# Performance work log

Hardware: AMD Instinct MI355X
Metric: run time of the kernel (lower is better)

## Reference

```python
import jax, jax.numpy as jnp
import numpy as np

N_TRAIN, D, B, N_CLASSES, K = 50000, 64, 128, 10, 16


def setup_inputs() -> dict:
    key = jax.random.key(0)
    k1, k2, k3 = jax.random.split(key, 3)
    train_data = jax.random.normal(k1, (N_TRAIN, D), dtype=jnp.float32)
    # one-hot class labels, as implied by gather -> sum over k -> argmax over classes
    labels = jax.random.randint(k2, (N_TRAIN,), 0, N_CLASSES)
    train_target = jax.nn.one_hot(labels, N_CLASSES, dtype=jnp.float32)
    x_test = jax.random.normal(k3, (B, D), dtype=jnp.float32)
    return {"train_data": train_data, "train_target": train_target,
            "x_test": x_test, "k": K}


def reference(train_data, train_target, x_test, k):
    # L1 (Manhattan) distance: [B, N_train]
    # broadcast: [1, N, D] - [B, 1, D] -> abs -> sum over D
    distance = jnp.sum(jnp.abs(train_data[None, :, :] - x_test[:, None, :]), axis=2)
    # top_k of negative distance == k nearest neighbors
    _, top_k_indices = jax.lax.top_k(-distance, k)          # [B, k]
    top_k_label = train_target[top_k_indices]               # [B, k, C] gather
    sum_up_predictions = jnp.sum(top_k_label, axis=1)       # [B, C] vote counts
    return jnp.argmax(sum_up_predictions, axis=1)           # [B] predicted class
```

## Files before the change

### kernel.cpp

```cpp
#include <hip/hip_runtime.h>
#include <cfloat>
#include <climits>
#include <stdint.h>

#define NTRAIN 50000
#define DIM 64
#define BQ 128
#define NCLS 10
#define KSEL 16
#define QPB 32
#define QG (BQ / QPB)
#define THREADS 256
#define TROWS 256
#define TPAD 68

__device__ __forceinline__ uint64_t pack_di(float d, int r) {
    return ((uint64_t)__float_as_uint(d) << 32) | (uint32_t)r;
}

__device__ __forceinline__ void ins16(uint64_t (&K)[KSEL], uint64_t pk) {
    if (pk < K[KSEL - 1]) {
        K[KSEL - 1] = pk;
#pragma unroll
        for (int j = KSEL - 1; j > 0; --j)
            if (K[j] < K[j - 1]) { uint64_t t = K[j]; K[j] = K[j - 1]; K[j - 1] = t; }
    }
}

__device__ __forceinline__ uint64_t adv16(const uint64_t (&K)[KSEL], int c) {
    uint64_t nh = ~0ULL;
#pragma unroll
    for (int q = 1; q < KSEL; ++q)
        if (c == q) nh = K[q];
    return nh;
}

__device__ __forceinline__ void wave_merge8(const uint64_t (&K)[KSEL], int rg, uint64_t* dst) {
    uint64_t h = K[0]; int c = 0;
#pragma unroll
    for (int r = 0; r < KSEL; ++r) {
        uint64_t m = h, o;
        o = __shfl_xor((unsigned long long)m, 1); if (o < m) m = o;
        o = __shfl_xor((unsigned long long)m, 2); if (o < m) m = o;
        o = __shfl_xor((unsigned long long)m, 4); if (o < m) m = o;
        if (m == h) { ++c; h = adv16(K, c); }
        if (rg == (r & 7)) dst[r] = m;
    }
}

__global__ __launch_bounds__(THREADS, 1) void knn_scan(
    const float* __restrict__ train, const float* __restrict__ xtest,
    uint64_t* __restrict__ cand, int S, int stripe_len)
{
    __shared__ float qs[QPB * TPAD];
    __shared__ __align__(16) float ts[TROWS * TPAD];

    const int bx     = blockIdx.x;
    const int stripe = bx % S;
    const int qgrp   = bx / S;
    const int q0     = qgrp * QPB;
    const int tid    = threadIdx.x;
    const int w      = tid >> 6;
    const int lane   = tid & 63;
    const int qg     = lane >> 3;
    const int rg     = lane & 7;

    const int r0 = stripe * stripe_len;
    const int r1 = min(NTRAIN, r0 + stripe_len);

    for (int f = tid; f < QPB * (DIM / 4); f += THREADS) {
        const int ql = f >> 4, c = f & 15;
        *(float4*)&qs[ql * TPAD + 4 * c] =
            *(const float4*)&xtest[(size_t)(q0 + ql) * DIM + 4 * c];
    }

    uint64_t k0[KSEL], k1[KSEL], k2[KSEL], k3[KSEL];
#pragma unroll
    for (int j = 0; j < KSEL; ++j) { k0[j] = ~0ULL; k1[j] = ~0ULL; k2[j] = ~0ULL; k3[j] = ~0ULL; }

    for (int base = r0; base < r1; base += TROWS) {
        const int nr = min(TROWS, r1 - base);
        __syncthreads();
        for (int f = tid; f < nr * (DIM / 4); f += THREADS) {
            const int r = f >> 4, c = f & 15;
            *(float4*)&ts[r * TPAD + 4 * c] =
                *(const float4*)&train[(size_t)(base + r) * DIM + 4 * c];
        }
        __syncthreads();

        float acc[4][8];
#pragma unroll
        for (int i = 0; i < 4; ++i)
#pragma unroll
            for (int j = 0; j < 8; ++j) acc[i][j] = 0.0f;

#pragma unroll 4
        for (int c = 0; c < DIM / 4; ++c) {
            float4 qv[4], tv[8];
#pragma unroll
            for (int i = 0; i < 4; ++i)
                qv[i] = *(const float4*)&qs[(qg + 8 * i) * TPAD + 4 * c];
#pragma unroll
            for (int j = 0; j < 8; ++j)
                tv[j] = *(const float4*)&ts[(w * 64 + rg + 8 * j) * TPAD + 4 * c];
#pragma unroll
            for (int i = 0; i < 4; ++i)
#pragma unroll
                for (int j = 0; j < 8; ++j) {
                    const float s01 = fabsf(tv[j].x - qv[i].x) + fabsf(tv[j].y - qv[i].y);
                    const float s23 = fabsf(tv[j].z - qv[i].z) + fabsf(tv[j].w - qv[i].w);
                    acc[i][j] += s01 + s23;
                }
        }

        const int rb = base + w * 64 + rg;
#pragma unroll
        for (int j = 0; j < 8; ++j) {
            const int r = rb + 8 * j;
            if (r < r1) {
                ins16(k0, pack_di(acc[0][j], r));
                ins16(k1, pack_di(acc[1][j], r));
                ins16(k2, pack_di(acc[2][j], r));
                ins16(k3, pack_di(acc[3][j], r));
            }
        }
    }

    __syncthreads();
    uint64_t* mg = (uint64_t*)ts;
    wave_merge8(k0, rg, &mg[((size_t)w * QPB + qg +  0) * 17]);
    wave_merge8(k1, rg, &mg[((size_t)w * QPB + qg +  8) * 17]);
    wave_merge8(k2, rg, &mg[((size_t)w * QPB + qg + 16) * 17]);
    wave_merge8(k3, rg, &mg[((size_t)w * QPB + qg + 24) * 17]);
    __syncthreads();

    if (tid < QPB) {
        uint64_t kk[KSEL];
#pragma unroll
        for (int j = 0; j < KSEL; ++j) kk[j] = ~0ULL;
        for (int v = 0; v < 4; ++v)
#pragma unroll
            for (int j = 0; j < KSEL; ++j)
                ins16(kk, mg[((size_t)v * QPB + tid) * 17 + j]);
#pragma unroll
        for (int j = 0; j < KSEL; ++j)
            cand[((size_t)(q0 + tid) * S + stripe) * KSEL + j] = kk[j];
    }
}

__global__ __launch_bounds__(64) void knn_final(
    const uint64_t* __restrict__ cand, const float* __restrict__ ttarget,
    int* __restrict__ out, int ncand)
{
    const int b = blockIdx.x, lane = threadIdx.x;

    uint64_t k[KSEL];
#pragma unroll
    for (int j = 0; j < KSEL; ++j) k[j] = ~0ULL;
    for (int c = lane; c < ncand; c += 64)
        ins16(k, cand[(size_t)b * ncand + c]);

    uint64_t h = k[0]; int c = 0;
    float v = 0.0f;
#pragma unroll
    for (int r = 0; r < KSEL; ++r) {
        uint64_t m = h, o;
#pragma unroll
        for (int sh = 1; sh < 64; sh <<= 1) {
            o = __shfl_xor((unsigned long long)m, sh);
            if (o < m) m = o;
        }
        if (m == h) { ++c; h = adv16(k, c); }
        const int wi = (int)(uint32_t)(m & 0xFFFFFFFFu);
        if (lane < NCLS) v += ttarget[(size_t)wi * NCLS + lane];
    }

    float bv = (lane < NCLS) ? v : -1.0f;
    int   bc = lane;
#pragma unroll
    for (int sh = 1; sh < 64; sh <<= 1) {
        const float xv = __shfl_xor(bv, sh);
        const int   xc = __shfl_xor(bc, sh);
        if (xv > bv || (xv == bv && xc < bc)) { bv = xv; bc = xc; }
    }
    if (lane == 0) out[b] = bc;
}

extern "C" void kernel_launch(void* const* d_in, const int* in_sizes, int n_in,
                              void* d_out, int out_size, void* d_ws, size_t ws_size,
                              hipStream_t stream) {
    const float* train   = (const float*)d_in[0];
    const float* ttarget = (const float*)d_in[1];
    const float* xtest   = (const float*)d_in[2];
    int* out = (int*)d_out;

    int S = 64;
    while (S > 8 && (size_t)BQ * S * KSEL * 8 > ws_size) S >>= 1;
    const int stripe_len = (NTRAIN + S - 1) / S;

    uint64_t* cand = (uint64_t*)d_ws;

    hipLaunchKernelGGL(knn_scan, dim3(QG * S), dim3(THREADS), 0, stream,
                       train, xtest, cand, S, stripe_len);
    hipLaunchKernelGGL(knn_final, dim3(BQ), dim3(64), 0, stream,
                       cand, ttarget, out, S * KSEL);
}
```

Baseline: 142.9 us.

## Prefilter top-k insertions with sampled distance threshold and double block size

Adds a pre-pass kernel that computes each query's 16th-smallest L1 distance over the first 1024 training rows and uses it (plus a margin) as a per-query threshold. The main scan then only runs the sorted insertion for candidates below that threshold, cutting the divergent insertion-sort cost. It also doubles threads and tile rows per block to 512, with two blocks per CU, and fixes the stripe count at 64. The threshold is exact because it comes from real distances, so at least 16 rows always pass, but the change adds a serial pre-kernel launch and uses more shared memory per block.

```diff
diff --git a/kernel.cpp b/kernel.cpp
--- a/kernel.cpp
+++ b/kernel.cpp
@@ -10,9 +10,12 @@
 #define KSEL 16
 #define QPB 32
 #define QG (BQ / QPB)
-#define THREADS 256
-#define TROWS 256
+#define THREADS 512
+#define TROWS 512
 #define TPAD 68
+#define NSAMP 1024
+#define SSTRIPES 64
+#define MARGIN 1e-2f
 
 __device__ __forceinline__ uint64_t pack_di(float d, int r) {
     return ((uint64_t)__float_as_uint(d) << 32) | (uint32_t)r;
@@ -48,16 +51,62 @@
     }
 }
 
-__global__ __launch_bounds__(THREADS, 1) void knn_scan(
+__global__ __launch_bounds__(64) void knn_tau(
     const float* __restrict__ train, const float* __restrict__ xtest,
-    uint64_t* __restrict__ cand, int S, int stripe_len)
+    float* __restrict__ tau)
+{
+    const int q = blockIdx.x, lane = threadIdx.x;
+
+    float4 qv[DIM / 4];
+    {
+        const float* qp = xtest + (size_t)q * DIM;
+#pragma unroll
+        for (int c = 0; c < DIM / 4; ++c) qv[c] = *(const float4*)(qp + 4 * c);
+    }
+
+    uint64_t K[KSEL];
+#pragma unroll
+    for (int j = 0; j < KSEL; ++j) K[j] = ~0ULL;
+
+    for (int t = 0; t < NSAMP / 64; ++t) {
+        const int r = lane + 64 * t;
+        const float* rp = train + (size_t)r * DIM;
+        float acc = 0.0f;
+#pragma unroll
+        for (int c = 0; c < DIM / 4; ++c) {
+            const float4 tv = *(const float4*)(rp + 4 * c);
+            const float s01 = fabsf(tv.x - qv[c].x) + fabsf(tv.y - qv[c].y);
+            const float s23 = fabsf(tv.z - qv[c].z) + fabsf(tv.w - qv[c].w);
+            acc += s01 + s23;
+        }
+        ins16(K, pack_di(acc, r));
+    }
+
+    uint64_t h = K[0]; int c = 0; uint64_t last = ~0ULL;
+#pragma unroll
+    for (int r = 0; r < KSEL; ++r) {
+        uint64_t m = h, o;
+#pragma unroll
+        for (int sh = 1; sh < 64; sh <<= 1) {
+            o = __shfl_xor((unsigned long long)m, sh);
+            if (o < m) m = o;
+        }
+        if (m == h) { ++c; h = adv16(K, c); }
+        last = m;
+    }
+    if (lane == 0) tau[q] = __uint_as_float((uint32_t)(last >> 32)) + MARGIN;
+}
+
+__global__ __launch_bounds__(THREADS, 2) void knn_scan(
+    const float* __restrict__ train, const float* __restrict__ xtest,
+    const float* __restrict__ tau, uint64_t* __restrict__ cand, int stripe_len)
 {
     __shared__ float qs[QPB * TPAD];
     __shared__ __align__(16) float ts[TROWS * TPAD];
 
     const int bx     = blockIdx.x;
-    const int stripe = bx % S;
-    const int qgrp   = bx / S;
+    const int stripe = bx % SSTRIPES;
+    const int qgrp   = bx / SSTRIPES;
     const int q0     = qgrp * QPB;
     const int tid    = threadIdx.x;
     const int w      = tid >> 6;
@@ -73,6 +122,10 @@
         *(float4*)&qs[ql * TPAD + 4 * c] =
             *(const float4*)&xtest[(size_t)(q0 + ql) * DIM + 4 * c];
     }
+
+    float tauv[4];
+#pragma unroll
+    for (int i = 0; i < 4; ++i) tauv[i] = tau[q0 + qg + 8 * i];
 
     uint64_t k0[KSEL], k1[KSEL], k2[KSEL], k3[KSEL];
 #pragma unroll
@@ -118,10 +171,10 @@
         for (int j = 0; j < 8; ++j) {
             const int r = rb + 8 * j;
             if (r < r1) {
-                ins16(k0, pack_di(acc[0][j], r));
-                ins16(k1, pack_di(acc[1][j], r));
-                ins16(k2, pack_di(acc[2][j], r));
-                ins16(k3, pack_di(acc[3][j], r));
+                if (acc[0][j] <= tauv[0]) ins16(k0, pack_di(acc[0][j], r));
+                if (acc[1][j] <= tauv[1]) ins16(k1, pack_di(acc[1][j], r));
+                if (acc[2][j] <= tauv[2]) ins16(k2, pack_di(acc[2][j], r));
+                if (acc[3][j] <= tauv[3]) ins16(k3, pack_di(acc[3][j], r));
             }
         }
     }
@@ -138,13 +191,13 @@
         uint64_t kk[KSEL];
 #pragma unroll
         for (int j = 0; j < KSEL; ++j) kk[j] = ~0ULL;
-        for (int v = 0; v < 4; ++v)
+        for (int v = 0; v < 8; ++v)
 #pragma unroll
             for (int j = 0; j < KSEL; ++j)
                 ins16(kk, mg[((size_t)v * QPB + tid) * 17 + j]);
 #pragma unroll
         for (int j = 0; j < KSEL; ++j)
-            cand[((size_t)(q0 + tid) * S + stripe) * KSEL + j] = kk[j];
+            cand[((size_t)(q0 + tid) * SSTRIPES + stripe) * KSEL + j] = kk[j];
     }
 }
 
@@ -194,14 +247,14 @@
     const float* xtest   = (const float*)d_in[2];
     int* out = (int*)d_out;
 
-    int S = 64;
-    while (S > 8 && (size_t)BQ * S * KSEL * 8 > ws_size) S >>= 1;
-    const int stripe_len = (NTRAIN + S - 1) / S;
-
-    uint64_t* cand = (uint64_t*)d_ws;
-
-    hipLaunchKernelGGL(knn_scan, dim3(QG * S), dim3(THREADS), 0, stream,
-                       train, xtest, cand, S, stripe_len);
+    const int stripe_len = (NTRAIN + SSTRIPES - 1) / SSTRIPES;
+
+    float*    tau  = (float*)d_ws;
+    uint64_t* cand = (uint64_t*)((char*)d_ws + 512);
+
+    hipLaunchKernelGGL(knn_tau, dim3(BQ), dim3(64), 0, stream, train, xtest, tau);
+    hipLaunchKernelGGL(knn_scan, dim3(QG * SSTRIPES), dim3(THREADS), 0, stream,
+                       train, xtest, tau, cand, stripe_len);
     hipLaunchKernelGGL(knn_final, dim3(BQ), dim3(64), 0, stream,
-                       cand, ttarget, out, S * KSEL);
-}
+                       cand, ttarget, out, SSTRIPES * KSEL);
+}
```

After: 138.8 us. 2.9% less time.
